# Optimization experiments

Measured on AMD Instinct MI355X. Metric: run time of the kernel, lower is better.

The kernel has to match this reference:

```python
import jax, jax.numpy as jnp
import numpy as np

N_NODES = 50000
N_EDGES = 800000
F_DIM = 128   # float_feat_dim
H_DIM = 64    # hidden_dim
NEG_SLOPE = 0.2


def setup_inputs() -> dict:
    key = jax.random.key(0)
    ks = jax.random.split(key, 12)
    in_dim = F_DIM + 1
    sc_in = 1.0 / np.sqrt(in_dim)
    sc_h = 1.0 / np.sqrt(H_DIM)
    return {
        "x_float": jax.random.normal(ks[0], (N_NODES, F_DIM), dtype=jnp.float32),
        "x_binary": jax.random.uniform(ks[1], (N_NODES,), dtype=jnp.float32),
        "edge_index": jax.random.randint(ks[2], (2, N_EDGES), 0, N_NODES, dtype=jnp.int64),
        "Wl": jax.random.normal(ks[3], (H_DIM, in_dim), dtype=jnp.float32) * sc_in,
        "bl": jnp.zeros((H_DIM,), dtype=jnp.float32),
        "Wr": jax.random.normal(ks[4], (H_DIM, in_dim), dtype=jnp.float32) * sc_in,
        "br": jnp.zeros((H_DIM,), dtype=jnp.float32),
        "att": jax.random.normal(ks[5], (H_DIM,), dtype=jnp.float32) * sc_h,
        "gat_bias": jnp.zeros((H_DIM,), dtype=jnp.float32),
        "Wo": jax.random.normal(ks[6], (F_DIM, H_DIM), dtype=jnp.float32) * sc_h,
        "bo": jnp.zeros((F_DIM,), dtype=jnp.float32),
        "dispersion": jnp.zeros((F_DIM,), dtype=jnp.float32),
    }


def reference(x_float, x_binary, edge_index, Wl, bl, Wr, br, att, gat_bias, Wo, bo, dispersion):
    N = x_float.shape[0]
    # concat float feats with binary feature -> [N, F+1]
    x = jnp.concatenate([x_float, x_binary[:, None]], axis=1)
    # add self loops (PyG GATv2Conv default)
    loops = jnp.arange(N, dtype=edge_index.dtype)
    src = jnp.concatenate([edge_index[0], loops])  # [E+N]
    dst = jnp.concatenate([edge_index[1], loops])
    # separate source/target linear projections (share_weights=False)
    xl = x @ Wl.T + bl  # [N, H]
    xr = x @ Wr.T + br  # [N, H]
    # per-edge GATv2 attention score: a^T LeakyReLU(x_l[j] + x_r[i])
    m = xl[src] + xr[dst]                      # [E+N, H]
    m = jnp.where(m > 0, m, NEG_SLOPE * m)
    e = m @ att                                # [E+N]
    # segment softmax over destination neighborhoods
    emax = jax.ops.segment_max(e, dst, num_segments=N)  # self loops => every seg nonempty
    ex = jnp.exp(e - emax[dst])
    denom = jax.ops.segment_sum(ex, dst, num_segments=N)
    alpha = ex / denom[dst]                    # [E+N]
    # weighted scatter-aggregate of source projections
    out = jax.ops.segment_sum(alpha[:, None] * xl[src], dst, num_segments=N) + gat_bias
    h = jax.nn.elu(out)                        # [N, H]
    logits = h @ Wo.T + bo                     # [N, F]
    return logits, jax.nn.softplus(dispersion)
```

## Files before the change

### kernel.cpp

```cpp
#include <hip/hip_runtime.h>
#include <hip/hip_bf16.h>
#include <math.h>

#define N_NODES 50000
#define N_EDGES 800000
#define F_DIM 128
#define H_DIM 64
#define IN_DIM 129
#define ETOT (N_EDGES + N_NODES)
#define PROJ_BLKS ((N_NODES + 31) / 32)
#define OUT_BLKS  ((N_NODES + 31) / 32)
#define NB 196
#define CAP 6144
#define EPB2 782
#define BKT_BLKS 1024

typedef __hip_bfloat16 bf16;
typedef __attribute__((ext_vector_type(8))) short bf16x8;
typedef __attribute__((ext_vector_type(4))) float f32x4;

static __device__ __forceinline__ float bs2f(short s) {
    union { float f; unsigned u; } c; c.u = ((unsigned)(unsigned short)s) << 16; return c.f;
}
static __device__ __forceinline__ short f2bs(float f) {
    union { bf16 b; short s; } u; u.b = __float2bfloat16(f); return u.s;
}

__global__ __launch_bounds__(256) void prep_kernel(
    const float* __restrict__ Wl, const float* __restrict__ Wr,
    const float* __restrict__ Wo,
    bf16* __restrict__ whi, bf16* __restrict__ wlo,
    bf16* __restrict__ wohi, bf16* __restrict__ wolo,
    int* __restrict__ gcur)
{
    int b = blockIdx.x, t = threadIdx.x;
    if (b < 8) {
        int s = b * 256 + t;
        int fid = s >> 6, l = s & 63;
        int wave = fid >> 3, nt = (fid >> 2) & 1, ks = fid & 3;
        int ch = wave * 32 + nt * 16 + (l & 15);
        int kb = ks * 32 + (l >> 4) * 8;
        const float* wrow = (ch < 64) ? Wl + (size_t)ch * IN_DIM
                                      : Wr + (size_t)(ch - 64) * IN_DIM;
        #pragma unroll
        for (int j = 0; j < 8; ++j) {
            float v = wrow[kb + j];
            short hs = f2bs(v);
            short ls = f2bs(v - bs2f(hs));
            ((short*)whi)[(size_t)s * 8 + j] = hs;
            ((short*)wlo)[(size_t)s * 8 + j] = ls;
        }
    } else if (b < 12) {
        int s = (b - 8) * 256 + t;
        int fid = s >> 6, l = s & 63;
        int wave = fid >> 2, nt = (fid >> 1) & 1, ks = fid & 1;
        int ch = wave * 32 + nt * 16 + (l & 15);
        int kb = ks * 32 + (l >> 4) * 8;
        const float* wrow = Wo + (size_t)ch * H_DIM;
        #pragma unroll
        for (int j = 0; j < 8; ++j) {
            float v = wrow[kb + j];
            short hs = f2bs(v);
            short ls = f2bs(v - bs2f(hs));
            ((short*)wohi)[(size_t)s * 8 + j] = hs;
            ((short*)wolo)[(size_t)s * 8 + j] = ls;
        }
    } else {
        if (t < NB) gcur[t] = 0;
    }
}

__global__ __launch_bounds__(256) void h1_kernel(
    const float* __restrict__ xf, const float* __restrict__ xb,
    const float* __restrict__ Wl, const float* __restrict__ bl,
    const float* __restrict__ Wr, const float* __restrict__ br,
    const bf16* __restrict__ whi, const bf16* __restrict__ wlo,
    const int* __restrict__ esrc, const int* __restrict__ edst,
    bf16* __restrict__ xl, bf16* __restrict__ xr,
    int* __restrict__ gcur, unsigned* __restrict__ bstore)
{
    __shared__ int smem[2048];

    if (blockIdx.x >= PROJ_BLKS) {
        unsigned* ent = (unsigned*)smem;
        int* hist  = smem + 782;
        int* lbase = smem + 978;
        int* c2    = smem + 1174;
        int t = threadIdx.x;
        if (t < NB) hist[t] = 0;
        __syncthreads();

        int e0 = (blockIdx.x - PROJ_BLKS) * EPB2;
        int cnt = N_EDGES - e0; if (cnt > EPB2) cnt = EPB2;
        for (int k = t; k < cnt; k += 256) {
            int dst = edst[e0 + k];
            ent[k] = ((unsigned)dst << 16) | (unsigned)esrc[e0 + k];
            atomicAdd(&hist[dst >> 8], 1);
        }
        __syncthreads();

        if (t < NB) {
            int hh = hist[t];
            lbase[t] = hh ? atomicAdd(&gcur[t], hh) : 0;
            c2[t] = 0;
        }
        __syncthreads();

        for (int k = t; k < cnt; k += 256) {
            unsigned en = ent[k];
            int j = en >> 24;
            int r = atomicAdd(&c2[j], 1);
            bstore[(size_t)j * CAP + lbase[j] + r] = en;
        }
        return;
    }

    short* lds = (short*)smem;

    int wave = threadIdx.x >> 6;
    int lane = threadIdx.x & 63;
    int n = lane & 15, q = lane >> 4;
    int node0 = blockIdx.x * 32;

    bf16x8 bhi[2][4], blo_[2][4];
    float biasv[2], w128[2];
    #pragma unroll
    for (int nt = 0; nt < 2; ++nt) {
        int ch = wave * 32 + nt * 16 + n;
        #pragma unroll
        for (int ks = 0; ks < 4; ++ks) {
            int fid = wave * 8 + nt * 4 + ks;
            bhi[nt][ks]  = *(const bf16x8*)(whi + ((size_t)fid * 64 + lane) * 8);
            blo_[nt][ks] = *(const bf16x8*)(wlo + ((size_t)fid * 64 + lane) * 8);
        }
        biasv[nt] = (ch < 64) ? bl[ch] : br[ch - 64];
        w128[nt]  = (ch < 64) ? Wl[(size_t)ch * IN_DIM + 128]
                              : Wr[(size_t)(ch - 64) * IN_DIM + 128];
    }

    #pragma unroll
    for (int mt = 0; mt < 2; ++mt) {
        int nb = node0 + mt * 16;
        if (nb < N_NODES) {
            const float* xrow = xf + (size_t)(nb + n) * F_DIM;
            bf16x8 a[4];
            #pragma unroll
            for (int ks = 0; ks < 4; ++ks) {
                float4 u = *(const float4*)(xrow + ks * 32 + q * 8);
                float4 v = *(const float4*)(xrow + ks * 32 + q * 8 + 4);
                bf16x8 tt;
                tt[0] = f2bs(u.x); tt[1] = f2bs(u.y); tt[2] = f2bs(u.z); tt[3] = f2bs(u.w);
                tt[4] = f2bs(v.x); tt[5] = f2bs(v.y); tt[6] = f2bs(v.z); tt[7] = f2bs(v.w);
                a[ks] = tt;
            }
            f32x4 acc[2] = {{0.f,0.f,0.f,0.f},{0.f,0.f,0.f,0.f}};
            #pragma unroll
            for (int ks = 0; ks < 4; ++ks) {
                #pragma unroll
                for (int nt = 0; nt < 2; ++nt) {
                    acc[nt] = __builtin_amdgcn_mfma_f32_16x16x32_bf16(a[ks], bhi[nt][ks],  acc[nt], 0, 0, 0);
                    acc[nt] = __builtin_amdgcn_mfma_f32_16x16x32_bf16(a[ks], blo_[nt][ks], acc[nt], 0, 0, 0);
                }
            }
            float4 xbv = *(const float4*)(xb + nb + q * 4);
            float xbr[4] = {xbv.x, xbv.y, xbv.z, xbv.w};
            #pragma unroll
            for (int nt = 0; nt < 2; ++nt) {
                int ch = wave * 32 + nt * 16 + n;
                int blk = ch >> 3, pos = ch & 7;
                #pragma unroll
                for (int r = 0; r < 4; ++r) {
                    int nodeL = mt * 16 + q * 4 + r;
                    float val = acc[nt][r] + xbr[r] * w128[nt] + biasv[nt];
                    lds[nodeL * 128 + ((blk ^ (nodeL & 7)) << 3) + pos] = f2bs(val);
                }
            }
        }
    }
    __syncthreads();

    int nl = threadIdx.x >> 3, bk = threadIdx.x & 7;
    int node = node0 + nl;
    if (node < N_NODES) {
        bf16x8 v0 = *(const bf16x8*)(lds + nl * 128 + ((bk ^ (nl & 7)) << 3));
        *(bf16x8*)(xl + (size_t)node * H_DIM + bk * 8) = v0;
        bf16x8 v1 = *(const bf16x8*)(lds + nl * 128 + (((8 + bk) ^ (nl & 7)) << 3));
        *(bf16x8*)(xr + (size_t)node * H_DIM + bk * 8) = v1;
    }
}

__global__ __launch_bounds__(512) void csr_kernel(
    const int* __restrict__ gcur, const unsigned* __restrict__ bstore,
    int* __restrict__ offs, int* __restrict__ csr_src)
{
    __shared__ unsigned ent[CAP];
    __shared__ int sh[256], h256[256], start[256], c2[256];
    __shared__ int bb_s, C_s;
    int j = blockIdx.x, t = threadIdx.x;

    int val = 0;
    if (t < NB) val = gcur[t] + ((t < NB - 1) ? 256 : (N_NODES - (NB - 1) * 256));
    if (t < 256) sh[t] = val;
    __syncthreads();
    #pragma unroll
    for (int d = 1; d < 256; d <<= 1) {
        int x = (t >= d && t < 256) ? sh[t - d] : 0;
        __syncthreads();
        if (t < 256) sh[t] += x;
        __syncthreads();
    }
    if (t == j) bb_s = sh[t] - val;
    if (t == 0) C_s = gcur[j];
    if (t < 256) h256[t] = 0;
    __syncthreads();
    int bb = bb_s, C = C_s;

    for (int k = t; k < C; k += 512) {
        unsigned en = bstore[(size_t)j * CAP + k];
        ent[k] = en;
        atomicAdd(&h256[(en >> 16) & 255], 1);
    }
    __syncthreads();

    int w = 0;
    if (t < 256) {
        w = h256[t] + ((j * 256 + t < N_NODES) ? 1 : 0);
        sh[t] = w;
    }
    __syncthreads();
    #pragma unroll
    for (int d = 1; d < 256; d <<= 1) {
        int x = (t >= d && t < 256) ? sh[t - d] : 0;
        __syncthreads();
        if (t < 256) sh[t] += x;
        __syncthreads();
    }
    if (t < 256) {
        int st = bb + sh[t] - w;
        start[t] = st;
        c2[t] = 0;
        int node = j * 256 + t;
        if (node < N_NODES) {
            offs[node] = st;
            csr_src[st] = node;
        }
    }
    if (j == NB - 1 && t == 0) offs[N_NODES] = ETOT;
    __syncthreads();

    for (int k = t; k < C; k += 512) {
        unsigned en = ent[k];
        int bin = (en >> 16) & 255;
        int r = atomicAdd(&c2[bin], 1);
        csr_src[start[bin] + 1 + r] = (int)(en & 0xffffu);
    }
}

__global__ __launch_bounds__(256) void agg_fused(
    const int* __restrict__ csr_src, const int* __restrict__ offs,
    const bf16* __restrict__ xl, const bf16* __restrict__ xr,
    const float* __restrict__ att, const float* __restrict__ gb,
    bf16* __restrict__ h)
{
    int wid  = (blockIdx.x * 256 + threadIdx.x) >> 6;
    int lane = threadIdx.x & 63;
    if (wid >= N_NODES) return;
    int g  = lane >> 3;
    int c8 = lane & 7;

    float attv[8], xrv[8];
    {
        bf16x8 xrow = *(const bf16x8*)(xr + (size_t)wid * H_DIM + c8 * 8);
        float4 a0 = *(const float4*)(att + c8 * 8);
        float4 a1 = *(const float4*)(att + c8 * 8 + 4);
        attv[0] = a0.x; attv[1] = a0.y; attv[2] = a0.z; attv[3] = a0.w;
        attv[4] = a1.x; attv[5] = a1.y; attv[6] = a1.z; attv[7] = a1.w;
        #pragma unroll
        for (int j = 0; j < 8; ++j) xrv[j] = bs2f(xrow[j]);
    }

    int beg = offs[wid];
    int end = offs[wid + 1];
    int last = end - 1;
    float den = 0.f;
    float acc[8] = {0.f, 0.f, 0.f, 0.f, 0.f, 0.f, 0.f, 0.f};

    int i0 = beg + g;        i0 = (i0 < end) ? i0 : last;
    int i1 = beg + 8 + g;    i1 = (i1 < end) ? i1 : last;
    int i2 = beg + 16 + g;   i2 = (i2 < end) ? i2 : last;
    int srcC = csr_src[i2];
    bf16x8 xa = *(const bf16x8*)(xl + (size_t)csr_src[i0] * H_DIM + c8 * 8);
    bf16x8 xb = *(const bf16x8*)(xl + (size_t)csr_src[i1] * H_DIM + c8 * 8);

    for (int base = beg; base < end; base += 8) {
        int i3 = base + 24 + g;  i3 = (i3 < end) ? i3 : last;
        int srcD = csr_src[i3];
        bf16x8 xc = *(const bf16x8*)(xl + (size_t)srcC * H_DIM + c8 * 8);

        bool valid = (base + g) < end;
        float xv[8], p = 0.f;
        #pragma unroll
        for (int j = 0; j < 8; ++j) {
            xv[j] = bs2f(xa[j]);
            float m = xv[j] + xrv[j];
            m = (m > 0.f) ? m : 0.2f * m;
            p += m * attv[j];
        }
        p += __shfl_xor(p, 1);
        p += __shfl_xor(p, 2);
        p += __shfl_xor(p, 4);
        float ex = valid ? __expf(p) : 0.f;
        den += ex;
        #pragma unroll
        for (int j = 0; j < 8; ++j) acc[j] += ex * xv[j];

        xa = xb;
        xb = xc;
        srcC = srcD;
    }

    #pragma unroll
    for (int j = 0; j < 8; ++j) {
        acc[j] += __shfl_xor(acc[j], 8);
        acc[j] += __shfl_xor(acc[j], 16);
        acc[j] += __shfl_xor(acc[j], 32);
    }
    den += __shfl_xor(den, 8);
    den += __shfl_xor(den, 16);
    den += __shfl_xor(den, 32);

    if (g == 0) {
        float inv = 1.0f / den;
        float4 g0 = *(const float4*)(gb + c8 * 8);
        float4 g1 = *(const float4*)(gb + c8 * 8 + 4);
        float gbv[8] = {g0.x, g0.y, g0.z, g0.w, g1.x, g1.y, g1.z, g1.w};
        bf16x8 ov;
        #pragma unroll
        for (int j = 0; j < 8; ++j) {
            float v = acc[j] * inv + gbv[j];
            v = (v > 0.f) ? v : expm1f(v);
            ov[j] = f2bs(v);
        }
        *(bf16x8*)(h + (size_t)wid * H_DIM + c8 * 8) = ov;
    }
}

__global__ __launch_bounds__(256) void out_mfma(
    const bf16* __restrict__ h,
    const bf16* __restrict__ wohi, const bf16* __restrict__ wolo,
    const float* __restrict__ bo, const float* __restrict__ disp,
    float* __restrict__ out)
{
    if (blockIdx.x == 0 && threadIdx.x < F_DIM) {
        float d = disp[threadIdx.x];
        out[(size_t)N_NODES * F_DIM + threadIdx.x] = (d > 20.f) ? d : log1pf(__expf(d));
    }

    __shared__ float ldso[32 * 132];

    int wave = threadIdx.x >> 6;
    int lane = threadIdx.x & 63;
    int n = lane & 15, q = lane >> 4;
    int node0 = blockIdx.x * 32;

    bf16x8 bhi[2][2], blo_[2][2];
    float bov[2];
    #pragma unroll
    for (int nt = 0; nt < 2; ++nt) {
        int ch = wave * 32 + nt * 16 + n;
        #pragma unroll
        for (int ks = 0; ks < 2; ++ks) {
            int fid = wave * 4 + nt * 2 + ks;
            bhi[nt][ks]  = *(const bf16x8*)(wohi + ((size_t)fid * 64 + lane) * 8);
            blo_[nt][ks] = *(const bf16x8*)(wolo + ((size_t)fid * 64 + lane) * 8);
        }
        bov[nt] = bo[ch];
    }

    #pragma unroll
    for (int mt = 0; mt < 2; ++mt) {
        int nb = node0 + mt * 16;
        if (nb < N_NODES) {
            const bf16* hrow = h + (size_t)(nb + n) * H_DIM;
            bf16x8 a[2];
            #pragma unroll
            for (int ks = 0; ks < 2; ++ks)
                a[ks] = *(const bf16x8*)(hrow + ks * 32 + q * 8);
            f32x4 acc[2] = {{0.f,0.f,0.f,0.f},{0.f,0.f,0.f,0.f}};
            #pragma unroll
            for (int ks = 0; ks < 2; ++ks) {
                #pragma unroll
                for (int nt = 0; nt < 2; ++nt) {
                    acc[nt] = __builtin_amdgcn_mfma_f32_16x16x32_bf16(a[ks], bhi[nt][ks],  acc[nt], 0, 0, 0);
                    acc[nt] = __builtin_amdgcn_mfma_f32_16x16x32_bf16(a[ks], blo_[nt][ks], acc[nt], 0, 0, 0);
                }
            }
            #pragma unroll
            for (int nt = 0; nt < 2; ++nt) {
                int ch = wave * 32 + nt * 16 + n;
                #pragma unroll
                for (int r = 0; r < 4; ++r) {
                    int nodeL = mt * 16 + q * 4 + r;
                    ldso[nodeL * 132 + ch] = acc[nt][r] + bov[nt];
                }
            }
        }
    }
    __syncthreads();

    int nl = threadIdx.x >> 3, c = threadIdx.x & 7;
    int node = node0 + nl;
    if (node < N_NODES) {
        const float* srcp = ldso + nl * 132 + c * 16;
        float* dstp = out + (size_t)node * F_DIM + c * 16;
        #pragma unroll
        for (int i = 0; i < 4; ++i)
            *(float4*)(dstp + i * 4) = *(const float4*)(srcp + i * 4);
    }
}

extern "C" void kernel_launch(void* const* d_in, const int* in_sizes, int n_in,
                              void* d_out, int out_size, void* d_ws, size_t ws_size,
                              hipStream_t stream)
{
    const float* xf  = (const float*)d_in[0];
    const float* xb  = (const float*)d_in[1];
    const int*   ei  = (const int*)d_in[2];
    const float* Wl  = (const float*)d_in[3];
    const float* bl  = (const float*)d_in[4];
    const float* Wr  = (const float*)d_in[5];
    const float* br  = (const float*)d_in[6];
    const float* att = (const float*)d_in[7];
    const float* gb  = (const float*)d_in[8];
    const float* Wo  = (const float*)d_in[9];
    const float* bo  = (const float*)d_in[10];
    const float* dp  = (const float*)d_in[11];
    float* out = (float*)d_out;
    const int* esrc = ei;
    const int* edst = ei + N_EDGES;

    char* ws = (char*)d_ws;
    const size_t SZB = (size_t)N_NODES * H_DIM * sizeof(bf16);
    bf16*  xl      = (bf16*)(ws);
    bf16*  xr      = (bf16*)(ws + SZB);
    bf16*  h       = (bf16*)(ws + 2 * SZB);
    unsigned* bstore = (unsigned*)h;
    int*   csr_src = (int*)(ws + 3 * SZB);
    int*   offs    = (int*)(ws + 3 * SZB + (size_t)ETOT * 4);
    int*   gcur    = offs + (N_NODES + 4);
    bf16*  whi     = (bf16*)(gcur + NB + 12);
    bf16*  wlo     = whi + 16384;
    bf16*  wohi    = wlo + 16384;
    bf16*  wolo    = wohi + 8192;

    prep_kernel<<<13, 256, 0, stream>>>(Wl, Wr, Wo, whi, wlo, wohi, wolo, gcur);

    h1_kernel<<<PROJ_BLKS + BKT_BLKS, 256, 0, stream>>>(
        xf, xb, Wl, bl, Wr, br, whi, wlo, esrc, edst, xl, xr, gcur, bstore);

    csr_kernel<<<NB, 512, 0, stream>>>(gcur, bstore, offs, csr_src);

    agg_fused<<<(N_NODES * 64) / 256, 256, 0, stream>>>(csr_src, offs,
                                                        xl, xr, att, gb, h);

    out_mfma<<<OUT_BLKS, 256, 0, stream>>>(h, wohi, wolo, bo, dp, out);
}
```

Before: 198.0 us.

## Replace global atomic bucket scatter with per-block sorted runs and offset table

The edge bucketing pass stops reserving slots in global per-bucket buffers with global atomics. Instead, 256 blocks each sort their 3125 edges locally by bucket into a contiguous region and record each bucket's offset and count in a transposed table. The CSR kernel then collects each bucket's pieces from all 256 blocks into shared memory using that table. This removes contention on the global cursors and makes the writes contiguous per block, but the gather in the CSR kernel becomes 256 serial per-thread copy loops, and fewer, larger bucketing blocks run.

```diff
diff --git a/kernel.cpp b/kernel.cpp
--- a/kernel.cpp
+++ b/kernel.cpp
@@ -12,8 +12,8 @@
 #define OUT_BLKS  ((N_NODES + 31) / 32)
 #define NB 196
 #define CAP 6144
-#define EPB2 782
-#define BKT_BLKS 1024
+#define EPB 3125
+#define BKT_BLKS 256
 
 typedef __hip_bfloat16 bf16;
 typedef __attribute__((ext_vector_type(8))) short bf16x8;
@@ -31,7 +31,7 @@
     const float* __restrict__ Wo,
     bf16* __restrict__ whi, bf16* __restrict__ wlo,
     bf16* __restrict__ wohi, bf16* __restrict__ wolo,
-    int* __restrict__ gcur)
+    int* __restrict__ gtot)
 {
     int b = blockIdx.x, t = threadIdx.x;
     if (b < 8) {
@@ -66,7 +66,7 @@
             ((short*)wolo)[(size_t)s * 8 + j] = ls;
         }
     } else {
-        if (t < NB) gcur[t] = 0;
+        if (t < NB) gtot[t] = 0;
     }
 }
 
@@ -77,40 +77,61 @@
     const bf16* __restrict__ whi, const bf16* __restrict__ wlo,
     const int* __restrict__ esrc, const int* __restrict__ edst,
     bf16* __restrict__ xl, bf16* __restrict__ xr,
-    int* __restrict__ gcur, unsigned* __restrict__ bstore)
+    int* __restrict__ gtot, unsigned* __restrict__ bstore2,
+    int* __restrict__ bofsT)
 {
     __shared__ int smem[2048];
 
     if (blockIdx.x >= PROJ_BLKS) {
-        unsigned* ent = (unsigned*)smem;
-        int* hist  = smem + 782;
-        int* lbase = smem + 978;
-        int* c2    = smem + 1174;
+        int* hist = smem;
+        int* base = smem + 256;
+        int* cur  = smem + 512;
+        int* shs  = smem + 768;
         int t = threadIdx.x;
+        int b = blockIdx.x - PROJ_BLKS;
+        int e0 = b * EPB;
         if (t < NB) hist[t] = 0;
         __syncthreads();
 
-        int e0 = (blockIdx.x - PROJ_BLKS) * EPB2;
-        int cnt = N_EDGES - e0; if (cnt > EPB2) cnt = EPB2;
-        for (int k = t; k < cnt; k += 256) {
-            int dst = edst[e0 + k];
-            ent[k] = ((unsigned)dst << 16) | (unsigned)esrc[e0 + k];
-            atomicAdd(&hist[dst >> 8], 1);
-        }
-        __syncthreads();
-
+        int myd[13]; int mys[13];
+        #pragma unroll
+        for (int i = 0; i < 13; ++i) {
+            int k = t + i * 256;
+            bool v = k < EPB;
+            int dst = v ? edst[e0 + k] : -1;
+            int sc  = v ? esrc[e0 + k] : 0;
+            myd[i] = dst; mys[i] = sc;
+            if (v) atomicAdd(&hist[dst >> 8], 1);
+        }
+        __syncthreads();
+
+        int hv = (t < NB) ? hist[t] : 0;
+        shs[t] = hv;
+        __syncthreads();
+        #pragma unroll
+        for (int d = 1; d < 256; d <<= 1) {
+            int x = (t >= d) ? shs[t - d] : 0;
+            __syncthreads();
+            shs[t] += x;
+            __syncthreads();
+        }
         if (t < NB) {
-            int hh = hist[t];
-            lbase[t] = hh ? atomicAdd(&gcur[t], hh) : 0;
-            c2[t] = 0;
-        }
-        __syncthreads();
-
-        for (int k = t; k < cnt; k += 256) {
-            unsigned en = ent[k];
-            int j = en >> 24;
-            int r = atomicAdd(&c2[j], 1);
-            bstore[(size_t)j * CAP + lbase[j] + r] = en;
+            int bs = shs[t] - hv;
+            base[t] = bs;
+            cur[t] = 0;
+            if (hv) atomicAdd(&gtot[t], hv);
+            bofsT[t * 256 + b] = (bs << 16) | hv;
+        }
+        __syncthreads();
+
+        #pragma unroll
+        for (int i = 0; i < 13; ++i) {
+            if (myd[i] >= 0) {
+                int j = myd[i] >> 8;
+                int slot = base[j] + atomicAdd(&cur[j], 1);
+                bstore2[(size_t)e0 + slot] =
+                    ((unsigned)myd[i] << 16) | (unsigned)mys[i];
+            }
         }
         return;
     }
@@ -190,17 +211,24 @@
 }
 
 __global__ __launch_bounds__(512) void csr_kernel(
-    const int* __restrict__ gcur, const unsigned* __restrict__ bstore,
+    const int* __restrict__ gtot, const unsigned* __restrict__ bstore2,
+    const int* __restrict__ bofsT,
     int* __restrict__ offs, int* __restrict__ csr_src)
 {
     __shared__ unsigned ent[CAP];
-    __shared__ int sh[256], h256[256], start[256], c2[256];
+    __shared__ int sh[256], gb_[256], bcnt_[256], bbase_[256];
+    __shared__ int h256[256], start[256], c2[256];
     __shared__ int bb_s, C_s;
     int j = blockIdx.x, t = threadIdx.x;
 
-    int val = 0;
-    if (t < NB) val = gcur[t] + ((t < NB - 1) ? 256 : (N_NODES - (NB - 1) * 256));
-    if (t < 256) sh[t] = val;
+    int bcnt = 0;
+    if (t < 256) {
+        unsigned v = (unsigned)bofsT[j * 256 + t];
+        bbase_[t] = (int)(v >> 16);
+        bcnt = (int)(v & 0xffffu);
+        bcnt_[t] = bcnt;
+        sh[t] = bcnt;
+    }
     __syncthreads();
     #pragma unroll
     for (int d = 1; d < 256; d <<= 1) {
@@ -209,17 +237,37 @@
         if (t < 256) sh[t] += x;
         __syncthreads();
     }
+    if (t < 256) gb_[t] = sh[t] - bcnt;
+    if (t == 255) C_s = sh[255];
+    __syncthreads();
+    int C = C_s;
+
+    if (t < 256) {
+        const unsigned* p = bstore2 + (size_t)t * EPB + bbase_[t];
+        int o = gb_[t];
+        int c = bcnt_[t];
+        for (int i = 0; i < c; ++i) ent[o + i] = p[i];
+    }
+    __syncthreads();
+
+    int val = 0;
+    if (t < NB) val = gtot[t] + ((t < NB - 1) ? 256 : (N_NODES - (NB - 1) * 256));
+    if (t < 256) sh[t] = val;
+    __syncthreads();
+    #pragma unroll
+    for (int d = 1; d < 256; d <<= 1) {
+        int x = (t >= d && t < 256) ? sh[t - d] : 0;
+        __syncthreads();
+        if (t < 256) sh[t] += x;
+        __syncthreads();
+    }
     if (t == j) bb_s = sh[t] - val;
-    if (t == 0) C_s = gcur[j];
     if (t < 256) h256[t] = 0;
     __syncthreads();
-    int bb = bb_s, C = C_s;
-
-    for (int k = t; k < C; k += 512) {
-        unsigned en = bstore[(size_t)j * CAP + k];
-        ent[k] = en;
-        atomicAdd(&h256[(en >> 16) & 255], 1);
-    }
+    int bb = bb_s;
+
+    for (int k = t; k < C; k += 512)
+        atomicAdd(&h256[(ent[k] >> 16) & 255], 1);
     __syncthreads();
 
     int w = 0;
@@ -444,21 +492,23 @@
     bf16*  xl      = (bf16*)(ws);
     bf16*  xr      = (bf16*)(ws + SZB);
     bf16*  h       = (bf16*)(ws + 2 * SZB);
-    unsigned* bstore = (unsigned*)h;
+    unsigned* bstore2 = (unsigned*)h;
     int*   csr_src = (int*)(ws + 3 * SZB);
     int*   offs    = (int*)(ws + 3 * SZB + (size_t)ETOT * 4);
-    int*   gcur    = offs + (N_NODES + 4);
-    bf16*  whi     = (bf16*)(gcur + NB + 12);
+    int*   gtot    = offs + (N_NODES + 4);
+    int*   bofsT   = gtot + 208;
+    bf16*  whi     = (bf16*)(bofsT + NB * 256);
     bf16*  wlo     = whi + 16384;
     bf16*  wohi    = wlo + 16384;
     bf16*  wolo    = wohi + 8192;
 
-    prep_kernel<<<13, 256, 0, stream>>>(Wl, Wr, Wo, whi, wlo, wohi, wolo, gcur);
+    prep_kernel<<<13, 256, 0, stream>>>(Wl, Wr, Wo, whi, wlo, wohi, wolo, gtot);
 
     h1_kernel<<<PROJ_BLKS + BKT_BLKS, 256, 0, stream>>>(
-        xf, xb, Wl, bl, Wr, br, whi, wlo, esrc, edst, xl, xr, gcur, bstore);
-
-    csr_kernel<<<NB, 512, 0, stream>>>(gcur, bstore, offs, csr_src);
+        xf, xb, Wl, bl, Wr, br, whi, wlo, esrc, edst, xl, xr,
+        gtot, bstore2, bofsT);
+
+    csr_kernel<<<NB, 512, 0, stream>>>(gtot, bstore2, bofsT, offs, csr_src);
 
     agg_fused<<<(N_NODES * 64) / 256, 256, 0, stream>>>(csr_src, offs,
                                                         xl, xr, att, gb, h);
```

After: 186.0 us. 1.06x faster.
